# Performance work log

Hardware: AMD Instinct MI355X
Metric: run time of the kernel (lower is better)

## Reference

```python
import jax, jax.numpy as jnp
import numpy as np

H = 5          # num_heads
QHD = 32       # query/key head dim
PHD = 4        # pos head dim


def setup_inputs() -> dict:
    key = jax.random.key(0)
    ks = jax.random.split(key, 8)
    T, B, D, PD = 512, 64, 512, 192
    lm_pruned = jax.random.normal(ks[0], (T, B, D), jnp.float32)
    am_pruned = jax.random.normal(ks[1], (T, B, D), jnp.float32)
    pos_emb = jax.random.normal(ks[2], (1, 2 * T - 1, PD), jnp.float32)
    key_padding_mask = jnp.zeros((B, T), bool)
    scale_q = QHD ** (-0.25)
    W_lm = (jax.random.normal(ks[3], (D, (QHD + PHD) * H), jnp.float32) * (scale_q / np.sqrt(D))).astype(jnp.float32)
    b_lm = jnp.zeros(((QHD + PHD) * H,), jnp.float32)
    W_am = (jax.random.normal(ks[4], (D, QHD * H), jnp.float32) * (scale_q / np.sqrt(D))).astype(jnp.float32)
    b_am = jnp.zeros((QHD * H,), jnp.float32)
    W_pos = (jax.random.normal(ks[5], (PD, H * PHD), jnp.float32) * (0.05 / np.sqrt(PD))).astype(jnp.float32)
    return {"lm_pruned": lm_pruned, "am_pruned": am_pruned, "pos_emb": pos_emb,
            "key_padding_mask": key_padding_mask,
            "W_lm": W_lm, "b_lm": b_lm, "W_am": W_am, "b_am": b_am, "W_pos": W_pos}


def reference(lm_pruned, am_pruned, pos_emb, key_padding_mask, W_lm, b_lm, W_am, b_am, W_pos):
    T, B, _ = lm_pruned.shape
    S = am_pruned.shape[0]
    lm = lm_pruned @ W_lm + b_lm          # (T, B, (QHD+PHD)*H)
    am = am_pruned @ W_am + b_am          # (S, B, QHD*H)
    q = lm[..., : H * QHD].reshape(T, B, H, QHD)
    p = lm[..., H * QHD:].reshape(T, B, H, PHD)
    k = am.reshape(S, B, H, QHD)          # whiten/balance are value-identity
    # content scores: (H, B, T, S)
    attn_scores = jnp.einsum('tbhd,sbhd->hbts', q, k)
    # positional scores
    pe = (pos_emb[0] @ W_pos).reshape(2 * T - 1, H, PHD)   # (2T-1, H, PHD)
    pos_scores = jnp.einsum('tbhd,nhd->hbtn', p, pe)        # (H, B, T, 2T-1)
    # Transformer-XL rel-shift: out[..., i, j] = pos_scores[..., i, j - i + T - 1]
    idx = jnp.arange(T)[None, :] - jnp.arange(T)[:, None] + (T - 1)  # (T, T)
    shifted = jnp.take_along_axis(pos_scores, idx[None, None, :, :], axis=-1)  # (H,B,T,T)
    attn_scores = attn_scores + shifted
    # key padding mask: (B, S) -> broadcast over heads and query positions
    attn_scores = jnp.where(key_padding_mask[None, :, None, :], jnp.float32(-1000.0), attn_scores)
    return jax.nn.softmax(attn_scores, axis=-1)
```

## Files before the change

kernel.cpp:

```cpp
#include <hip/hip_runtime.h>

#define TT 512
#define BB 64
#define HH 5
#define NPOS 1023

typedef __bf16 bf16x8 __attribute__((ext_vector_type(8)));
typedef __bf16 bf16x4 __attribute__((ext_vector_type(4)));
typedef float floatx4 __attribute__((ext_vector_type(4)));

__global__ void prep_kernel(const float* __restrict__ Wlm, const float* __restrict__ Wam,
                            const float* __restrict__ pos_emb, const float* __restrict__ Wpos,
                            __bf16* __restrict__ WlmT, __bf16* __restrict__ WamT,
                            __bf16* __restrict__ peB) {
  int bx = blockIdx.x;
  if (bx < 384) {
    int idx = bx * 256 + threadIdx.x;
    if (idx < 192 * 512) {
      int n = idx >> 9, k = idx & 511;
      float v = (n < 180) ? Wlm[k * 180 + n] : 0.f;
      WlmT[idx] = (__bf16)v;
    }
    if (idx < 160 * 512) {
      int n = idx >> 9, k = idx & 511;
      WamT[idx] = (__bf16)Wam[k * 160 + n];
    }
  } else {
    int t = (bx - 384) * 256 + threadIdx.x;
    int n = t >> 5, c = t & 31;
    if (n < NPOS && c < 20) {
      float acc = 0.f;
#pragma unroll 8
      for (int pd = 0; pd < 192; ++pd) acc += pos_emb[n * 192 + pd] * Wpos[pd * 20 + c];
      int h = c >> 2, d = c & 3;
      peB[((size_t)h * NPOS + n) * 4 + d] = (__bf16)acc;
    }
  }
}

template <int NT, bool IS_LM>
__device__ __forceinline__ void proj_body(const float* __restrict__ A, const __bf16* __restrict__ WT,
                                          const float* __restrict__ bias, __bf16* __restrict__ qk_out,
                                          float* __restrict__ p_out, int blk,
                                          __bf16 (*a_lds)[32], __bf16 (*w_lds)[32]) {
  const int tid = threadIdx.x;
  const int m0 = blk * 64;
  const int lane = tid & 63, w = tid >> 6;
  const int quad = lane >> 4, nl = lane & 15;

  floatx4 acc[NT];
#pragma unroll
  for (int j = 0; j < NT; ++j) acc[j] = floatx4{0.f, 0.f, 0.f, 0.f};

  const int arow = tid >> 2, aseg = tid & 3;
  for (int k0 = 0; k0 < 512; k0 += 32) {
    const float* ap = A + (size_t)(m0 + arow) * 512 + k0 + aseg * 8;
    float4 av0 = *(const float4*)ap;
    float4 av1 = *(const float4*)(ap + 4);
    bf16x8 pk;
    pk[0] = (__bf16)av0.x; pk[1] = (__bf16)av0.y; pk[2] = (__bf16)av0.z; pk[3] = (__bf16)av0.w;
    pk[4] = (__bf16)av1.x; pk[5] = (__bf16)av1.y; pk[6] = (__bf16)av1.z; pk[7] = (__bf16)av1.w;
    *(bf16x8*)&a_lds[arow][aseg * 8] = pk;
#pragma unroll
    for (int task = tid; task < NT * 64; task += 256) {
      int n = task >> 2, seg = task & 3;
      *(bf16x8*)&w_lds[n][seg * 8] = *(const bf16x8*)(WT + (size_t)n * 512 + k0 + seg * 8);
    }
    __syncthreads();
    bf16x8 afr = *(const bf16x8*)&a_lds[16 * w + nl][quad * 8];
#pragma unroll
    for (int jt = 0; jt < NT; ++jt) {
      bf16x8 bfr = *(const bf16x8*)&w_lds[jt * 16 + nl][quad * 8];
      acc[jt] = __builtin_amdgcn_mfma_f32_16x16x32_bf16(afr, bfr, acc[jt], 0, 0, 0);
    }
    __syncthreads();
  }
#pragma unroll
  for (int jt = 0; jt < NT; ++jt) {
    int c = jt * 16 + nl;
#pragma unroll
    for (int r = 0; r < 4; ++r) {
      int m = m0 + 16 * w + quad * 4 + r;
      float bv = IS_LM ? ((c < 180) ? bias[c] : 0.f) : bias[c];
      float val = acc[jt][r] + bv;
      if (IS_LM) {
        if (c < 160) qk_out[(size_t)m * 160 + c] = (__bf16)val;
        else if (c < 180) p_out[(size_t)m * 20 + (c - 160)] = val;
      } else {
        qk_out[(size_t)m * 160 + c] = (__bf16)val;
      }
    }
  }
}

__global__ __launch_bounds__(256, 4) void proj_kernel(
    const float* __restrict__ lm, const __bf16* __restrict__ WlmT, const float* __restrict__ blm,
    __bf16* __restrict__ qbuf, float* __restrict__ pbuf,
    const float* __restrict__ am, const __bf16* __restrict__ WamT, const float* __restrict__ bam,
    __bf16* __restrict__ kbuf) {
  __shared__ __align__(16) __bf16 a_lds[64][32];
  __shared__ __align__(16) __bf16 w_lds[192][32];
  if (blockIdx.x < 512)
    proj_body<12, true>(lm, WlmT, blm, qbuf, pbuf, blockIdx.x, a_lds, w_lds);
  else
    proj_body<10, false>(am, WamT, bam, kbuf, nullptr, blockIdx.x - 512, a_lds, w_lds);
}

__global__ __launch_bounds__(256, 2) void attn_kernel(
    const __bf16* __restrict__ q, const __bf16* __restrict__ k,
    const float* __restrict__ p, const __bf16* __restrict__ peB,
    const unsigned char* __restrict__ mask, float* __restrict__ out) {
  __shared__ __align__(16) __bf16 k_lds[512][32];
  __shared__ __align__(16) __bf16 q_lds[64][32];
  __shared__ __align__(16) float p_lds[64][4];
  __shared__ __align__(16) __bf16 pe_lds[576 * 4];
  __shared__ float mask_lds[512];

  const int tid = threadIdx.x;
  const int t0 = blockIdx.x * 64;
  const int b = blockIdx.y;
  const int h = blockIdx.z;
  const int lane = tid & 63, w = tid >> 6;
  const int quad = lane >> 4, nl = lane & 15;

#pragma unroll
  for (int it = 0; it < 8; ++it) {
    int idx = tid + it * 256;
    int s = idx >> 2, c = idx & 3;
    *(bf16x8*)&k_lds[s][c * 8] =
        *(const bf16x8*)(k + (size_t)(s * BB + b) * 160 + h * 32 + c * 8);
  }
  {
    int s = tid >> 2, c = tid & 3;
    *(bf16x8*)&q_lds[s][c * 8] =
        *(const bf16x8*)(q + (size_t)((t0 + s) * BB + b) * 160 + h * 32 + c * 8);
  }
  if (tid < 64)
    *(float4*)&p_lds[tid][0] = *(const float4*)(p + (size_t)((t0 + tid) * BB + b) * 20 + h * 4);
  {
    int u0 = 448 - t0;
    for (int i = tid; i < 575; i += 256)
      *(bf16x4*)&pe_lds[i * 4] = *(const bf16x4*)(peB + ((size_t)h * NPOS + u0 + i) * 4);
  }
  for (int i = tid; i < 512; i += 256)
    mask_lds[i] = mask[b * 512 + i] ? -1000.f : 0.f;
  __syncthreads();

  floatx4 acc[32];
  bf16x8 af = *(const bf16x8*)&q_lds[16 * w + nl][quad * 8];
#pragma unroll
  for (int jt = 0; jt < 32; ++jt) {
    float m = mask_lds[jt * 16 + nl];
    floatx4 cin = {m, m, m, m};
    bf16x8 bfr = *(const bf16x8*)&k_lds[jt * 16 + nl][quad * 8];
    acc[jt] = __builtin_amdgcn_mfma_f32_16x16x32_bf16(af, bfr, cin, 0, 0, 0);
  }

  const int base = 16 * w + quad * 4;
  floatx4 pv[4];
#pragma unroll
  for (int r = 0; r < 4; ++r) pv[r] = *(const floatx4*)&p_lds[base + r][0];

  const uint32_t* pp = (const uint32_t*)pe_lds + 2 * (nl - base + 63);
  float mx[4] = {-3.4e38f, -3.4e38f, -3.4e38f, -3.4e38f};
#pragma unroll
  for (int jt = 0; jt < 32; ++jt) {
    const uint32_t* pj = pp + jt * 32;
#pragma unroll
    for (int r = 0; r < 4; ++r) {
      uint32_t w0 = pj[-2 * r], w1 = pj[1 - 2 * r];
      float f0 = __uint_as_float(w0 << 16);
      float f1 = __uint_as_float(w0 & 0xffff0000u);
      float f2 = __uint_as_float(w1 << 16);
      float f3 = __uint_as_float(w1 & 0xffff0000u);
      float v = acc[jt][r];
      v = fmaf(pv[r][0], f0, v);
      v = fmaf(pv[r][1], f1, v);
      v = fmaf(pv[r][2], f2, v);
      v = fmaf(pv[r][3], f3, v);
      acc[jt][r] = v;
      mx[r] = fmaxf(mx[r], v);
    }
  }

#pragma unroll
  for (int r = 0; r < 4; ++r) {
#pragma unroll
    for (int d = 1; d < 16; d <<= 1) mx[r] = fmaxf(mx[r], __shfl_xor(mx[r], d, 64));
  }
  float rinv[4];
#pragma unroll
  for (int r = 0; r < 4; ++r) {
    float sum = 0.f;
#pragma unroll
    for (int jt = 0; jt < 32; ++jt) {
      float e = __expf(acc[jt][r] - mx[r]);
      acc[jt][r] = e;
      sum += e;
    }
#pragma unroll
    for (int d = 1; d < 16; d <<= 1) sum += __shfl_xor(sum, d, 64);
    rinv[r] = 1.0f / sum;
  }
#pragma unroll
  for (int r = 0; r < 4; ++r) {
    size_t basep = (((size_t)h * BB + b) * TT + (t0 + base + r)) * TT;
#pragma unroll
    for (int jt = 0; jt < 32; ++jt) out[basep + jt * 16 + nl] = acc[jt][r] * rinv[r];
  }
}

extern "C" void kernel_launch(void* const* d_in, const int* in_sizes, int n_in,
                              void* d_out, int out_size, void* d_ws, size_t ws_size,
                              hipStream_t stream) {
  const float* lm = (const float*)d_in[0];
  const float* am = (const float*)d_in[1];
  const float* pos_emb = (const float*)d_in[2];
  const unsigned char* mask = (const unsigned char*)d_in[3];
  const float* Wlm = (const float*)d_in[4];
  const float* blm = (const float*)d_in[5];
  const float* Wam = (const float*)d_in[6];
  const float* bam = (const float*)d_in[7];
  const float* Wpos = (const float*)d_in[8];
  float* out = (float*)d_out;

  char* ws = (char*)d_ws;
  __bf16* qbuf = (__bf16*)ws;
  __bf16* kbuf = qbuf + (size_t)32768 * 160;
  float* pbuf = (float*)(kbuf + (size_t)32768 * 160);
  __bf16* peB = (__bf16*)(pbuf + (size_t)32768 * 20);
  __bf16* WlmT = peB + (size_t)5 * 1024 * 4;
  __bf16* WamT = WlmT + (size_t)192 * 512;

  prep_kernel<<<512, 256, 0, stream>>>(Wlm, Wam, pos_emb, Wpos, WlmT, WamT, peB);
  proj_kernel<<<1024, 256, 0, stream>>>(lm, WlmT, blm, qbuf, pbuf, am, WamT, bam, kbuf);
  attn_kernel<<<dim3(8, BB, HH), 256, 0, stream>>>(qbuf, kbuf, pbuf, peB, mask, out);
}
```

Measured before the change: 511.9 us.

## Transpose MFMA operands so each lane owns a query row and writes vectorized outputs

Swaps the A/B operands of the MFMA in both the projection and attention kernels. Each lane now holds four consecutive columns of one row, so the outputs can go out as float4 and bf16x4 stores instead of scattered scalar stores. The softmax row reductions shrink to two cross-quad shuffles. The positional table is kept in fp32 with float4 LDS reads instead of packed bf16 unpacking, which doubles its LDS footprint and global traffic.

After: 525.5 us. 1.03x slower.

```diff
diff --git a/kernel.cpp b/kernel.cpp
--- a/kernel.cpp
+++ b/kernel.cpp
@@ -12,7 +12,7 @@
 __global__ void prep_kernel(const float* __restrict__ Wlm, const float* __restrict__ Wam,
                             const float* __restrict__ pos_emb, const float* __restrict__ Wpos,
                             __bf16* __restrict__ WlmT, __bf16* __restrict__ WamT,
-                            __bf16* __restrict__ peB) {
+                            float* __restrict__ peF) {
   int bx = blockIdx.x;
   if (bx < 384) {
     int idx = bx * 256 + threadIdx.x;
@@ -33,7 +33,7 @@
 #pragma unroll 8
       for (int pd = 0; pd < 192; ++pd) acc += pos_emb[n * 192 + pd] * Wpos[pd * 20 + c];
       int h = c >> 2, d = c & 3;
-      peB[((size_t)h * NPOS + n) * 4 + d] = (__bf16)acc;
+      peF[((size_t)h * NPOS + n) * 4 + d] = acc;
     }
   }
 }
@@ -71,24 +71,28 @@
 #pragma unroll
     for (int jt = 0; jt < NT; ++jt) {
       bf16x8 bfr = *(const bf16x8*)&w_lds[jt * 16 + nl][quad * 8];
-      acc[jt] = __builtin_amdgcn_mfma_f32_16x16x32_bf16(afr, bfr, acc[jt], 0, 0, 0);
+      acc[jt] = __builtin_amdgcn_mfma_f32_16x16x32_bf16(bfr, afr, acc[jt], 0, 0, 0);
     }
     __syncthreads();
   }
+  const int m = m0 + 16 * w + nl;
 #pragma unroll
   for (int jt = 0; jt < NT; ++jt) {
-    int c = jt * 16 + nl;
-#pragma unroll
-    for (int r = 0; r < 4; ++r) {
-      int m = m0 + 16 * w + quad * 4 + r;
-      float bv = IS_LM ? ((c < 180) ? bias[c] : 0.f) : bias[c];
-      float val = acc[jt][r] + bv;
-      if (IS_LM) {
-        if (c < 160) qk_out[(size_t)m * 160 + c] = (__bf16)val;
-        else if (c < 180) p_out[(size_t)m * 20 + (c - 160)] = val;
-      } else {
-        qk_out[(size_t)m * 160 + c] = (__bf16)val;
-      }
+    const int c0 = jt * 16 + quad * 4;
+    if (!IS_LM || c0 < 160) {
+      float4 bv = *(const float4*)(bias + c0);
+      bf16x4 o;
+      o[0] = (__bf16)(acc[jt][0] + bv.x);
+      o[1] = (__bf16)(acc[jt][1] + bv.y);
+      o[2] = (__bf16)(acc[jt][2] + bv.z);
+      o[3] = (__bf16)(acc[jt][3] + bv.w);
+      *(bf16x4*)(qk_out + (size_t)m * 160 + c0) = o;
+    } else if (c0 < 180) {
+      float4 bv = *(const float4*)(bias + c0);
+      float4 o;
+      o.x = acc[jt][0] + bv.x; o.y = acc[jt][1] + bv.y;
+      o.z = acc[jt][2] + bv.z; o.w = acc[jt][3] + bv.w;
+      *(float4*)(p_out + (size_t)m * 20 + (c0 - 160)) = o;
     }
   }
 }
@@ -108,12 +112,12 @@
 
 __global__ __launch_bounds__(256, 2) void attn_kernel(
     const __bf16* __restrict__ q, const __bf16* __restrict__ k,
-    const float* __restrict__ p, const __bf16* __restrict__ peB,
+    const float* __restrict__ p, const float* __restrict__ peF,
     const unsigned char* __restrict__ mask, float* __restrict__ out) {
   __shared__ __align__(16) __bf16 k_lds[512][32];
   __shared__ __align__(16) __bf16 q_lds[64][32];
   __shared__ __align__(16) float p_lds[64][4];
-  __shared__ __align__(16) __bf16 pe_lds[576 * 4];
+  __shared__ __align__(16) float pe_lds[576 * 4];
   __shared__ float mask_lds[512];
 
   const int tid = threadIdx.x;
@@ -140,73 +144,70 @@
   {
     int u0 = 448 - t0;
     for (int i = tid; i < 575; i += 256)
-      *(bf16x4*)&pe_lds[i * 4] = *(const bf16x4*)(peB + ((size_t)h * NPOS + u0 + i) * 4);
+      *(float4*)&pe_lds[i * 4] = *(const float4*)(peF + ((size_t)h * NPOS + u0 + i) * 4);
   }
   for (int i = tid; i < 512; i += 256)
     mask_lds[i] = mask[b * 512 + i] ? -1000.f : 0.f;
   __syncthreads();
 
   floatx4 acc[32];
-  bf16x8 af = *(const bf16x8*)&q_lds[16 * w + nl][quad * 8];
-#pragma unroll
-  for (int jt = 0; jt < 32; ++jt) {
-    float m = mask_lds[jt * 16 + nl];
-    floatx4 cin = {m, m, m, m};
-    bf16x8 bfr = *(const bf16x8*)&k_lds[jt * 16 + nl][quad * 8];
-    acc[jt] = __builtin_amdgcn_mfma_f32_16x16x32_bf16(af, bfr, cin, 0, 0, 0);
-  }
-
-  const int base = 16 * w + quad * 4;
-  floatx4 pv[4];
-#pragma unroll
-  for (int r = 0; r < 4; ++r) pv[r] = *(const floatx4*)&p_lds[base + r][0];
-
-  const uint32_t* pp = (const uint32_t*)pe_lds + 2 * (nl - base + 63);
+  bf16x8 bq = *(const bf16x8*)&q_lds[16 * w + nl][quad * 8];
+#pragma unroll
+  for (int jt = 0; jt < 32; ++jt) {
+    floatx4 cin = *(const floatx4*)&mask_lds[jt * 16 + quad * 4];
+    bf16x8 ak = *(const bf16x8*)&k_lds[jt * 16 + nl][quad * 8];
+    acc[jt] = __builtin_amdgcn_mfma_f32_16x16x32_bf16(ak, bq, cin, 0, 0, 0);
+  }
+
+  const int tl = 16 * w + nl;
+  const floatx4 pv = *(const floatx4*)&p_lds[tl][0];
+  const int ibase = quad * 4 - tl + 63;
+  const floatx4* pef = (const floatx4*)pe_lds;
   float mx[4] = {-3.4e38f, -3.4e38f, -3.4e38f, -3.4e38f};
 #pragma unroll
   for (int jt = 0; jt < 32; ++jt) {
-    const uint32_t* pj = pp + jt * 32;
+    const int i0 = ibase + jt * 16;
+    floatx4 v = acc[jt];
 #pragma unroll
     for (int r = 0; r < 4; ++r) {
-      uint32_t w0 = pj[-2 * r], w1 = pj[1 - 2 * r];
-      float f0 = __uint_as_float(w0 << 16);
-      float f1 = __uint_as_float(w0 & 0xffff0000u);
-      float f2 = __uint_as_float(w1 << 16);
-      float f3 = __uint_as_float(w1 & 0xffff0000u);
-      float v = acc[jt][r];
-      v = fmaf(pv[r][0], f0, v);
-      v = fmaf(pv[r][1], f1, v);
-      v = fmaf(pv[r][2], f2, v);
-      v = fmaf(pv[r][3], f3, v);
-      acc[jt][r] = v;
-      mx[r] = fmaxf(mx[r], v);
-    }
-  }
-
-#pragma unroll
-  for (int r = 0; r < 4; ++r) {
-#pragma unroll
-    for (int d = 1; d < 16; d <<= 1) mx[r] = fmaxf(mx[r], __shfl_xor(mx[r], d, 64));
-  }
-  float rinv[4];
-#pragma unroll
-  for (int r = 0; r < 4; ++r) {
-    float sum = 0.f;
-#pragma unroll
-    for (int jt = 0; jt < 32; ++jt) {
-      float e = __expf(acc[jt][r] - mx[r]);
-      acc[jt][r] = e;
-      sum += e;
-    }
-#pragma unroll
-    for (int d = 1; d < 16; d <<= 1) sum += __shfl_xor(sum, d, 64);
-    rinv[r] = 1.0f / sum;
-  }
-#pragma unroll
-  for (int r = 0; r < 4; ++r) {
-    size_t basep = (((size_t)h * BB + b) * TT + (t0 + base + r)) * TT;
-#pragma unroll
-    for (int jt = 0; jt < 32; ++jt) out[basep + jt * 16 + nl] = acc[jt][r] * rinv[r];
+      floatx4 pe4 = pef[i0 + r];
+      float val = v[r];
+      val = fmaf(pv[0], pe4[0], val);
+      val = fmaf(pv[1], pe4[1], val);
+      val = fmaf(pv[2], pe4[2], val);
+      val = fmaf(pv[3], pe4[3], val);
+      v[r] = val;
+      mx[r] = fmaxf(mx[r], val);
+    }
+    acc[jt] = v;
+  }
+
+  float mxa = fmaxf(fmaxf(mx[0], mx[1]), fmaxf(mx[2], mx[3]));
+  mxa = fmaxf(mxa, __shfl_xor(mxa, 16, 64));
+  mxa = fmaxf(mxa, __shfl_xor(mxa, 32, 64));
+
+  float s0 = 0.f, s1 = 0.f, s2 = 0.f, s3 = 0.f;
+#pragma unroll
+  for (int jt = 0; jt < 32; ++jt) {
+    floatx4 v = acc[jt];
+    float e0 = __expf(v[0] - mxa);
+    float e1 = __expf(v[1] - mxa);
+    float e2 = __expf(v[2] - mxa);
+    float e3 = __expf(v[3] - mxa);
+    acc[jt] = floatx4{e0, e1, e2, e3};
+    s0 += e0; s1 += e1; s2 += e2; s3 += e3;
+  }
+  float sum = (s0 + s1) + (s2 + s3);
+  sum += __shfl_xor(sum, 16, 64);
+  sum += __shfl_xor(sum, 32, 64);
+  const float rinv = 1.0f / sum;
+
+  float* op = out + (((size_t)h * BB + b) * TT + (t0 + tl)) * TT + quad * 4;
+#pragma unroll
+  for (int jt = 0; jt < 32; ++jt) {
+    floatx4 v = acc[jt];
+    v[0] *= rinv; v[1] *= rinv; v[2] *= rinv; v[3] *= rinv;
+    *(floatx4*)(op + jt * 16) = v;
   }
 }
 
@@ -228,11 +229,11 @@
   __bf16* qbuf = (__bf16*)ws;
   __bf16* kbuf = qbuf + (size_t)32768 * 160;
   float* pbuf = (float*)(kbuf + (size_t)32768 * 160);
-  __bf16* peB = (__bf16*)(pbuf + (size_t)32768 * 20);
-  __bf16* WlmT = peB + (size_t)5 * 1024 * 4;
+  float* peF = pbuf + (size_t)32768 * 20;
+  __bf16* WlmT = (__bf16*)(peF + (size_t)5 * 1024 * 4);
   __bf16* WamT = WlmT + (size_t)192 * 512;
 
-  prep_kernel<<<512, 256, 0, stream>>>(Wlm, Wam, pos_emb, Wpos, WlmT, WamT, peB);
+  prep_kernel<<<512, 256, 0, stream>>>(Wlm, Wam, pos_emb, Wpos, WlmT, WamT, peF);
   proj_kernel<<<1024, 256, 0, stream>>>(lm, WlmT, blm, qbuf, pbuf, am, WamT, bam, kbuf);
-  attn_kernel<<<dim3(8, BB, HH), 256, 0, stream>>>(qbuf, kbuf, pbuf, peB, mask, out);
-}
+  attn_kernel<<<dim3(8, BB, HH), 256, 0, stream>>>(qbuf, kbuf, pbuf, peF, mask, out);
+}
```
